# Optimization experiments

Measured on AMD Instinct MI355X. Metric: run time of the kernel, lower is better.

Reference implementation:

```python
import jax, jax.numpy as jnp
import numpy as np

N, D, E, R, G, M = 8192, 1024, 64, 64, 8, 8

def setup_inputs() -> dict:
    key = jax.random.key(0)
    k_h, k_wg, k_wl, k_w1, k_w2 = jax.random.split(key, 5)
    return {
        'h': jax.random.normal(k_h, (N, D), jnp.float32),
        'Wg': jax.random.normal(k_wg, (D, G), jnp.float32) * 0.02,  # nn.Linear weight (transposed)
        'bg': jnp.zeros((G,), jnp.float32),
        'Wloc': jax.random.normal(k_wl, (G, D, M), jnp.float32) * 0.02,
        'W1': jax.random.normal(k_w1, (E, D, R), jnp.float32) * 0.02,
        'W2': jax.random.normal(k_w2, (E, R, D), jnp.float32) * 0.02,
        'k': 2,
    }

def reference(h, Wg, bg, Wloc, W1, W2, k):
    n, d = h.shape
    g, _, m = Wloc.shape
    e = W1.shape[0]
    router_temp = 1.0
    # stage 1: group routing (top-1)
    g_scores = h @ Wg + bg                                   # (N, G)
    group_idx = jnp.argmax(g_scores, axis=-1)                # (N,)
    # stage 2: within-group scores; compute all groups (cheap: N*G*M) then select
    all_local = jnp.einsum('nd,gdm->ngm', h, Wloc)           # (N, G, M)
    local_scores = jnp.take_along_axis(all_local, group_idx[:, None, None], axis=1)[:, 0]  # (N, M)
    topv, topm = jax.lax.top_k(local_scores, k)              # (N, k)
    gate = jax.nn.softmax(topv / max(router_temp, 1e-6), axis=-1)
    expert_ids = group_idx[:, None] * m + topm               # (N, k) global expert ids
    # scatter gates into dense (N, E); topm entries are distinct per token
    gate_full = jnp.zeros((n, e), h.dtype).at[jnp.arange(n)[:, None], expert_ids].set(gate)
    # low-rank expert compute: relu(h @ W1) @ W2, weighted-combined
    tmp = jax.nn.relu(jnp.einsum('nd,edr->ner', h, W1))      # (N, E, R)
    out = jnp.einsum('ner,erd->nd', gate_full[:, :, None] * tmp, W2)  # (N, D)
    return out, expert_ids, gate, group_idx
```

## Files before the change

kernel.cpp:

```cpp
#include <hip/hip_runtime.h>
#include <hip/hip_bf16.h>
#include <cstdint>
#include <cstddef>

#define NTOK 8192
#define DIM  1024
#define NEXP 64
#define RANK 64
#define NGRP 8
#define NLOC 8

typedef __attribute__((ext_vector_type(8))) short bf16x8;
typedef __attribute__((ext_vector_type(4))) float f32x4;

static __device__ inline unsigned int pack_bf16x2(float a, float b) {
    __hip_bfloat16 ha = __float2bfloat16(a);
    __hip_bfloat16 hb = __float2bfloat16(b);
    return (unsigned int)(*(unsigned short*)&ha) |
           ((unsigned int)(*(unsigned short*)&hb) << 16);
}

__global__ __launch_bounds__(256, 2) void score_all(
    const float* __restrict__ h, const float* __restrict__ Wg,
    const float* __restrict__ Wloc, unsigned short* __restrict__ hb,
    float* __restrict__ Sp)
{
    __shared__ float Hs[64][65];
    __shared__ float Ws[64][44];

    const int tile = blockIdx.x;
    const int slab = blockIdx.y;
    const int z    = blockIdx.z;
    const int tid  = threadIdx.x;
    const int wave = tid >> 6;
    const int lane = tid & 63;
    const int t0   = tile * 64;
    const int kz   = z * 512;
    const int ncol = slab ? 32 : 40;

    float acc[10] = {};

    for (int chunk = 0; chunk < 8; ++chunk) {
        const int kb = kz + chunk * 64;
        __syncthreads();
        {
            const int r = tid >> 2, seg = (tid & 3) * 16;
            const float* src = h + (size_t)(t0 + r) * DIM + kb + seg;
            const float4 v0 = *(const float4*)(src);
            const float4 v1 = *(const float4*)(src + 4);
            const float4 v2 = *(const float4*)(src + 8);
            const float4 v3 = *(const float4*)(src + 12);
            float* dst = &Hs[r][seg];
            dst[0]  = v0.x; dst[1]  = v0.y; dst[2]  = v0.z; dst[3]  = v0.w;
            dst[4]  = v1.x; dst[5]  = v1.y; dst[6]  = v1.z; dst[7]  = v1.w;
            dst[8]  = v2.x; dst[9]  = v2.y; dst[10] = v2.z; dst[11] = v2.w;
            dst[12] = v3.x; dst[13] = v3.y; dst[14] = v3.z; dst[15] = v3.w;
            if (slab == 0) {
                unsigned short* hrow = hb + (size_t)(t0 + r) * DIM + kb + seg;
                uint2 p0, p1, p2, p3;
                p0.x = pack_bf16x2(v0.x, v0.y); p0.y = pack_bf16x2(v0.z, v0.w);
                p1.x = pack_bf16x2(v1.x, v1.y); p1.y = pack_bf16x2(v1.z, v1.w);
                p2.x = pack_bf16x2(v2.x, v2.y); p2.y = pack_bf16x2(v2.z, v2.w);
                p3.x = pack_bf16x2(v3.x, v3.y); p3.y = pack_bf16x2(v3.z, v3.w);
                *(uint2*)(hrow)      = p0;
                *(uint2*)(hrow + 4)  = p1;
                *(uint2*)(hrow + 8)  = p2;
                *(uint2*)(hrow + 12) = p3;
            }
        }
        {
            const int krow = tid & 63;
            const int c4b  = tid >> 6;
#pragma unroll
            for (int p = 0; p < 3; ++p) {
                const int c4 = c4b + p * 4;
                if (c4 * 4 < ncol) {
                    const int o = c4 >> 1, m4 = (c4 & 1) * 4;
                    const float* wsrc;
                    if (slab == 0) {
                        wsrc = (o == 0)
                            ? (Wg + (size_t)(kb + krow) * NGRP + m4)
                            : (Wloc + (size_t)(o - 1) * (DIM * NLOC)
                                    + (size_t)(kb + krow) * NLOC + m4);
                    } else {
                        wsrc = Wloc + (size_t)(4 + o) * (DIM * NLOC)
                                    + (size_t)(kb + krow) * NLOC + m4;
                    }
                    *(float4*)&Ws[krow][c4 * 4] = *(const float4*)wsrc;
                }
            }
        }
        __syncthreads();
        if (slab == 0) {
            const int c0 = wave * 10;
#pragma unroll 4
            for (int k = 0; k < 64; ++k) {
                const float a = Hs[lane][k];
                const float2 b0 = *(const float2*)&Ws[k][c0];
                const float2 b1 = *(const float2*)&Ws[k][c0 + 2];
                const float2 b2 = *(const float2*)&Ws[k][c0 + 4];
                const float2 b3 = *(const float2*)&Ws[k][c0 + 6];
                const float2 b4 = *(const float2*)&Ws[k][c0 + 8];
                acc[0] += a * b0.x; acc[1] += a * b0.y;
                acc[2] += a * b1.x; acc[3] += a * b1.y;
                acc[4] += a * b2.x; acc[5] += a * b2.y;
                acc[6] += a * b3.x; acc[7] += a * b3.y;
                acc[8] += a * b4.x; acc[9] += a * b4.y;
            }
        } else {
            const int c0 = wave * 8;
#pragma unroll 4
            for (int k = 0; k < 64; ++k) {
                const float a = Hs[lane][k];
                const float4 b0 = *(const float4*)&Ws[k][c0];
                const float4 b1 = *(const float4*)&Ws[k][c0 + 4];
                acc[0] += a * b0.x; acc[1] += a * b0.y;
                acc[2] += a * b0.z; acc[3] += a * b0.w;
                acc[4] += a * b1.x; acc[5] += a * b1.y;
                acc[6] += a * b1.z; acc[7] += a * b1.w;
            }
        }
    }
    const int gcol = (slab ? 40 + wave * 8 : wave * 10);
    float* dstS = Sp + (size_t)z * (NTOK * 72) + (size_t)(t0 + lane) * 72 + gcol;
    if (slab == 0) {
#pragma unroll
        for (int c = 0; c < 10; ++c) dstS[c] = acc[c];
    } else {
#pragma unroll
        for (int c = 0; c < 8; ++c) dstS[c] = acc[c];
    }
}

__global__ __launch_bounds__(256) void route_all(
    const float* __restrict__ Sp, const float* __restrict__ bg,
    float* __restrict__ out_gidx, float* __restrict__ out_eid,
    float* __restrict__ out_gate, int* __restrict__ ws_eids,
    float* __restrict__ ws_gates, int* __restrict__ counts_e)
{
    __shared__ int hist[NEXP];
    if (threadIdx.x < NEXP) hist[threadIdx.x] = 0;
    __syncthreads();

    const int t = blockIdx.x * 256 + threadIdx.x;
    const float* p0 = Sp + (size_t)t * 72;
    const float* p1 = Sp + (size_t)NTOK * 72 + (size_t)t * 72;
    float s[72];
#pragma unroll
    for (int i = 0; i < 18; ++i) {
        const float4 a = *(const float4*)(p0 + i * 4);
        const float4 b = *(const float4*)(p1 + i * 4);
        s[i * 4 + 0] = a.x + b.x; s[i * 4 + 1] = a.y + b.y;
        s[i * 4 + 2] = a.z + b.z; s[i * 4 + 3] = a.w + b.w;
    }

    int gi = 0; float best = s[0] + bg[0];
#pragma unroll
    for (int g = 1; g < NGRP; ++g) {
        const float v = s[g] + bg[g];
        if (v > best) { best = v; gi = g; }
    }

    float ls[NLOC];
#pragma unroll
    for (int m = 0; m < NLOC; ++m) ls[m] = s[8 + gi * NLOC + m];

    int m1 = 0; float v1 = ls[0];
#pragma unroll
    for (int m = 1; m < NLOC; ++m) { if (ls[m] > v1) { v1 = ls[m]; m1 = m; } }
    int m2 = (m1 == 0) ? 1 : 0; float v2 = ls[m2];
#pragma unroll
    for (int m = 0; m < NLOC; ++m) {
        if (m != m1 && m != ((m1 == 0) ? 1 : 0) && ls[m] > v2) { v2 = ls[m]; m2 = m; }
    }
    const float e2v = expf(v2 - v1);
    const float inv = 1.f / (1.f + e2v);
    const float g0 = inv, g1 = e2v * inv;
    const int ea = gi * NLOC + m1, eb = gi * NLOC + m2;

    out_gidx[t] = (float)gi;
    out_eid[t * 2 + 0] = (float)ea;
    out_eid[t * 2 + 1] = (float)eb;
    out_gate[t * 2 + 0] = g0;
    out_gate[t * 2 + 1] = g1;
    ws_eids[t * 2 + 0] = ea;
    ws_eids[t * 2 + 1] = eb;
    ws_gates[t * 2 + 0] = g0;
    ws_gates[t * 2 + 1] = g1;
    atomicAdd(&hist[ea], 1);
    atomicAdd(&hist[eb], 1);

    __syncthreads();
    if (threadIdx.x < NEXP) atomicAdd(&counts_e[threadIdx.x], hist[threadIdx.x]);
}

__global__ __launch_bounds__(256) void scatter_e(
    const int* __restrict__ ws_eids, const float* __restrict__ ws_gates,
    const int* __restrict__ counts_e, int* __restrict__ cursor,
    int* __restrict__ token_list, float* __restrict__ slot_gate)
{
    __shared__ int offS[64];
    const int tid = threadIdx.x;
    if (tid < 64) {
        const int c = counts_e[tid];
        int s = c;
#pragma unroll
        for (int d = 1; d < 64; d <<= 1) {
            int v = __shfl_up(s, d, 64);
            if (tid >= d) s += v;
        }
        offS[tid] = s - c;
    }
    __syncthreads();
    const int t = blockIdx.x * 256 + tid;
    if (t >= NTOK) return;
#pragma unroll
    for (int j = 0; j < 2; ++j) {
        const int eid = ws_eids[t * 2 + j];
        const int pos = offS[eid] + atomicAdd(&cursor[eid], 1);
        token_list[pos] = t * 2 + j;
        slot_gate[pos] = ws_gates[t * 2 + j];
    }
}

__global__ __launch_bounds__(256) void prep_w(
    const float* __restrict__ W1, const float* __restrict__ W2,
    unsigned short* __restrict__ W1t, unsigned short* __restrict__ W2t)
{
    __shared__ float Ls[64][65];
    const int e = blockIdx.x;
    const int y = blockIdx.y;
    if (y < 16) {
        const int kb = y;
        const float* src = W1 + (size_t)e * DIM * RANK + (size_t)kb * 64 * RANK;
#pragma unroll
        for (int it = 0; it < 4; ++it) {
            const int kk = (threadIdx.x >> 4) + it * 16;
            const int rr = (threadIdx.x & 15) * 4;
            *(float4*)&Ls[kk][rr] = *(const float4*)(src + (size_t)kk * RANK + rr);
        }
        __syncthreads();
#pragma unroll
        for (int it = 0; it < 2; ++it) {
            const int idx = threadIdx.x + it * 256;
            const int r = idx >> 3, k8 = (idx & 7) * 8;
            uint4 v;
            v.x = pack_bf16x2(Ls[k8 + 0][r], Ls[k8 + 1][r]);
            v.y = pack_bf16x2(Ls[k8 + 2][r], Ls[k8 + 3][r]);
            v.z = pack_bf16x2(Ls[k8 + 4][r], Ls[k8 + 5][r]);
            v.w = pack_bf16x2(Ls[k8 + 6][r], Ls[k8 + 7][r]);
            *(uint4*)(W1t + (size_t)e * RANK * DIM + (size_t)r * DIM + kb * 64 + k8) = v;
        }
    } else {
        const int db = y - 16;
        const float* src = W2 + (size_t)e * RANK * DIM + db * 64;
#pragma unroll
        for (int it = 0; it < 4; ++it) {
            const int rr = (threadIdx.x >> 4) + it * 16;
            const int dd = (threadIdx.x & 15) * 4;
            *(float4*)&Ls[rr][dd] = *(const float4*)(src + (size_t)rr * DIM + dd);
        }
        __syncthreads();
#pragma unroll
        for (int it = 0; it < 2; ++it) {
            const int idx = threadIdx.x + it * 256;
            const int d = idx >> 3, r8 = (idx & 7) * 8;
            uint4 v;
            v.x = pack_bf16x2(Ls[r8 + 0][d], Ls[r8 + 1][d]);
            v.y = pack_bf16x2(Ls[r8 + 2][d], Ls[r8 + 3][d]);
            v.z = pack_bf16x2(Ls[r8 + 4][d], Ls[r8 + 5][d]);
            v.w = pack_bf16x2(Ls[r8 + 6][d], Ls[r8 + 7][d]);
            *(uint4*)(W2t + (size_t)e * DIM * RANK + (size_t)(db * 64 + d) * RANK + r8) = v;
        }
    }
}

__global__ __launch_bounds__(256, 2) void e1_mfma(
    const unsigned short* __restrict__ hb, const unsigned short* __restrict__ W1t,
    const int* __restrict__ counts_e, const int* __restrict__ token_list,
    const float* __restrict__ slot_gate, unsigned short* __restrict__ P)
{
    __shared__ unsigned short Hs[64 * 72];
    __shared__ unsigned short Ws[64 * 72];
    __shared__ int   tokS[64];
    __shared__ float gateS[64];
    __shared__ int   offS[65];

    const int e   = blockIdx.x;
    const int tid = threadIdx.x;
    if (tid < 64) {
        const int c = counts_e[tid];
        int s = c;
#pragma unroll
        for (int d = 1; d < 64; d <<= 1) {
            int v = __shfl_up(s, d, 64);
            if (tid >= d) s += v;
        }
        offS[tid] = s - c;
        if (tid == 63) offS[64] = s;
    }
    __syncthreads();
    const int n0 = offS[e];
    const int ne = offS[e + 1] - n0;

    const unsigned short* W1te = W1t + (size_t)e * RANK * DIM;
    const int wave = tid >> 6;
    const int lane = tid & 63;
    const int tx   = lane & 15;
    const int quad = lane >> 4;

    for (int tile = blockIdx.y; tile * 64 < ne; tile += 8) {
        const int row0 = tile * 64;
        __syncthreads();
        if (tid < 64) {
            const int gr = row0 + tid;
            tokS[tid]  = (gr < ne) ? token_list[n0 + gr] : -1;
            gateS[tid] = (gr < ne) ? slot_gate[n0 + gr] : 0.f;
        }
        f32x4 acc[4] = {};
        for (int kc = 0; kc < DIM; kc += 64) {
            __syncthreads();
#pragma unroll
            for (int it = 0; it < 2; ++it) {
                const int idx = tid + it * 256;
                const int s = idx >> 3, k8 = (idx & 7) * 8;
                const int ent = tokS[s];
                uint4 v = make_uint4(0, 0, 0, 0);
                if (ent >= 0)
                    v = *(const uint4*)(hb + (size_t)(ent >> 1) * DIM + kc + k8);
                *(uint4*)(Hs + s * 72 + k8) = v;
            }
#pragma unroll
            for (int it = 0; it < 2; ++it) {
                const int idx = tid + it * 256;
                const int r = idx >> 3, k8 = (idx & 7) * 8;
                *(uint4*)(Ws + r * 72 + k8) =
                    *(const uint4*)(W1te + (size_t)r * DIM + kc + k8);
            }
            __syncthreads();
#pragma unroll
            for (int ks = 0; ks < 2; ++ks) {
                const bf16x8 a = *(const bf16x8*)(Hs + (wave * 16 + tx) * 72 + ks * 32 + quad * 8);
#pragma unroll
                for (int j = 0; j < 4; ++j) {
                    const bf16x8 b = *(const bf16x8*)(Ws + (j * 16 + tx) * 72 + ks * 32 + quad * 8);
                    acc[j] = __builtin_amdgcn_mfma_f32_16x16x32_bf16(a, b, acc[j], 0, 0, 0);
                }
            }
        }
#pragma unroll
        for (int j = 0; j < 4; ++j) {
#pragma unroll
            for (int i = 0; i < 4; ++i) {
                const int sl = wave * 16 + quad * 4 + i;
                const int gr = row0 + sl;
                if (gr < ne) {
                    const float v = fmaxf(acc[j][i], 0.f) * gateS[sl];
                    __hip_bfloat16 hv = __float2bfloat16(v);
                    P[(size_t)(n0 + gr) * RANK + j * 16 + tx] = *(unsigned short*)&hv;
                }
            }
        }
    }
}

__global__ __launch_bounds__(256, 2) void e2_mfma(
    const unsigned short* __restrict__ P, const unsigned short* __restrict__ W2t,
    const int* __restrict__ counts_e, const int* __restrict__ token_list,
    float* __restrict__ out, float* __restrict__ contrib)
{
    __shared__ unsigned short Ps[64 * 72];
    __shared__ unsigned short W2s[64 * 72];
    __shared__ int tokS[64];
    __shared__ int offS[65];

    const int e = blockIdx.x;
    const int colbase = blockIdx.y * 64;
    const int tid = threadIdx.x;
    if (tid < 64) {
        const int c = counts_e[tid];
        int s = c;
#pragma unroll
        for (int d = 1; d < 64; d <<= 1) {
            int v = __shfl_up(s, d, 64);
            if (tid >= d) s += v;
        }
        offS[tid] = s - c;
        if (tid == 63) offS[64] = s;
    }
    __syncthreads();
    const int n0 = offS[e];
    const int ne = offS[e + 1] - n0;

    const unsigned short* W2te = W2t + (size_t)e * DIM * RANK;
    const int wave = tid >> 6;
    const int lane = tid & 63;
    const int tx   = lane & 15;
    const int quad = lane >> 4;

#pragma unroll
    for (int it = 0; it < 2; ++it) {
        const int idx = tid + it * 256;
        const int d = idx >> 3, r8 = (idx & 7) * 8;
        *(uint4*)(W2s + d * 72 + r8) =
            *(const uint4*)(W2te + (size_t)(colbase + d) * RANK + r8);
    }

    for (int tile = blockIdx.z; tile * 64 < ne; tile += 4) {
        const int row0 = tile * 64;
        __syncthreads();
        if (tid < 64) {
            const int gr = row0 + tid;
            tokS[tid] = (gr < ne) ? token_list[n0 + gr] : -1;
        }
#pragma unroll
        for (int it = 0; it < 2; ++it) {
            const int idx = tid + it * 256;
            const int s = idx >> 3, r8 = (idx & 7) * 8;
            const int gr = row0 + s;
            uint4 v = make_uint4(0, 0, 0, 0);
            if (gr < ne) v = *(const uint4*)(P + (size_t)(n0 + gr) * RANK + r8);
            *(uint4*)(Ps + s * 72 + r8) = v;
        }
        __syncthreads();
        f32x4 acc[4] = {};
#pragma unroll
        for (int ks = 0; ks < 2; ++ks) {
            const bf16x8 a = *(const bf16x8*)(Ps + (wave * 16 + tx) * 72 + ks * 32 + quad * 8);
#pragma unroll
            for (int j = 0; j < 4; ++j) {
                const bf16x8 b = *(const bf16x8*)(W2s + (j * 16 + tx) * 72 + ks * 32 + quad * 8);
                acc[j] = __builtin_amdgcn_mfma_f32_16x16x32_bf16(a, b, acc[j], 0, 0, 0);
            }
        }
#pragma unroll
        for (int i = 0; i < 4; ++i) {
            const int sl = wave * 16 + quad * 4 + i;
            const int ent = tokS[sl];
            if (ent >= 0) {
                float* base = (ent & 1) ? contrib : out;
                float* op = base + (size_t)(ent >> 1) * DIM + colbase;
#pragma unroll
                for (int j = 0; j < 4; ++j)
                    op[j * 16 + tx] = acc[j][i];
            }
        }
    }
}

__global__ __launch_bounds__(256) void combine_kernel(
    const float* __restrict__ contrib, float* __restrict__ out)
{
    const size_t i = (size_t)blockIdx.x * 256 + threadIdx.x;
    float4 a = ((const float4*)out)[i];
    const float4 b = ((const float4*)contrib)[i];
    a.x += b.x; a.y += b.y; a.z += b.z; a.w += b.w;
    ((float4*)out)[i] = a;
}

extern "C" void kernel_launch(void* const* d_in, const int* in_sizes, int n_in,
                              void* d_out, int out_size, void* d_ws, size_t ws_size,
                              hipStream_t stream)
{
    const float* h    = (const float*)d_in[0];
    const float* Wg   = (const float*)d_in[1];
    const float* bg   = (const float*)d_in[2];
    const float* Wloc = (const float*)d_in[3];
    const float* W1   = (const float*)d_in[4];
    const float* W2   = (const float*)d_in[5];

    float* out_f    = (float*)d_out;
    float* out_main = out_f;
    float* out_eid  = out_f + (size_t)NTOK * DIM;
    float* out_gate = out_eid + (size_t)NTOK * 2;
    float* out_gidx = out_gate + (size_t)NTOK * 2;

    int* ws_i        = (int*)d_ws;
    int* counts_e    = ws_i;
    int* cursor_e    = ws_i + 192;
    int* ws_eids     = ws_i + 16896;
    int* token_list  = ws_i + 33280;
    float* ws_f      = (float*)(ws_i + 49664);
    float* ws_gates  = ws_f;
    float* slot_gate = ws_f + 16384;
    float* Sp        = ws_f + 2 * 16384;
    unsigned short* P_h = (unsigned short*)(Sp + (size_t)2 * NTOK * 72);
    unsigned short* W1t = P_h + (size_t)16384 * RANK;
    unsigned short* W2t = W1t + (size_t)NEXP * RANK * DIM;
    float* contrib      = (float*)(W2t + (size_t)NEXP * DIM * RANK);
    unsigned short* hb = (unsigned short*)contrib;

    hipMemsetAsync(ws_i, 0, 256 * sizeof(int), stream);

    prep_w<<<dim3(NEXP, 32), 256, 0, stream>>>(W1, W2, W1t, W2t);
    score_all<<<dim3(128, 2, 2), 256, 0, stream>>>(h, Wg, Wloc, hb, Sp);
    route_all<<<NTOK / 256, 256, 0, stream>>>(Sp, bg, out_gidx, out_eid,
        out_gate, ws_eids, ws_gates, counts_e);
    scatter_e<<<NTOK / 256, 256, 0, stream>>>(ws_eids, ws_gates, counts_e,
        cursor_e, token_list, slot_gate);
    e1_mfma<<<dim3(NEXP, 8), 256, 0, stream>>>(hb, W1t, counts_e, token_list,
        slot_gate, P_h);
    e2_mfma<<<dim3(NEXP, 16, 4), 256, 0, stream>>>(P_h, W2t, counts_e, token_list,
        out_main, contrib);
    combine_kernel<<<(NTOK * DIM / 4) / 256, 256, 0, stream>>>(contrib, out_main);
}
```

Before: 259.6 us.

## Double token tile in score kernel with register prefetch and transposed weight tile

The scoring kernel now handles 128 tokens per block instead of 64, so each weight value read from shared memory feeds two tokens. The weight tile is stored transposed so the inner loop reads four k values at once. The next chunk's h and weight values are prefetched into registers while the current chunk is computed. In exchange the grid has half as many blocks, register pressure rises (20 accumulators plus prefetch buffers), and the launch bound no longer asks for two blocks per CU, so occupancy may drop.

```diff
diff --git a/kernel.cpp b/kernel.cpp
--- a/kernel.cpp
+++ b/kernel.cpp
@@ -20,13 +20,13 @@
            ((unsigned int)(*(unsigned short*)&hb) << 16);
 }
 
-__global__ __launch_bounds__(256, 2) void score_all(
+__global__ __launch_bounds__(256) void score_all(
     const float* __restrict__ h, const float* __restrict__ Wg,
     const float* __restrict__ Wloc, unsigned short* __restrict__ hb,
     float* __restrict__ Sp)
 {
-    __shared__ float Hs[64][65];
-    __shared__ float Ws[64][44];
+    __shared__ float Hs[128][66];
+    __shared__ float Ws[40][72];
 
     const int tile = blockIdx.x;
     const int slab = blockIdx.y;
@@ -34,102 +34,207 @@
     const int tid  = threadIdx.x;
     const int wave = tid >> 6;
     const int lane = tid & 63;
-    const int t0   = tile * 64;
+    const int t0   = tile * 128;
     const int kz   = z * 512;
-    const int ncol = slab ? 32 : 40;
-
-    float acc[10] = {};
+
+    const int r0  = tid >> 2;
+    const int seg = (tid & 3) * 16;
+
+    float acc[20] = {};
+
+    float4 hpre[8];
+    float4 wgp;
+    float4 wlp[2];
+
+    {
+        const int kb = kz;
+#pragma unroll
+        for (int half = 0; half < 2; ++half) {
+            const float* src = h + (size_t)(t0 + half * 64 + r0) * DIM + kb + seg;
+            hpre[half * 4 + 0] = *(const float4*)(src);
+            hpre[half * 4 + 1] = *(const float4*)(src + 4);
+            hpre[half * 4 + 2] = *(const float4*)(src + 8);
+            hpre[half * 4 + 3] = *(const float4*)(src + 12);
+        }
+        if (slab == 0) {
+            if (tid < 128)
+                wgp = *(const float4*)(Wg + (size_t)(kb + (tid >> 1)) * NGRP + (tid & 1) * 4);
+#pragma unroll
+            for (int it = 0; it < 2; ++it) {
+                const int idx = tid + it * 256;
+                const int g = idx >> 7, r = idx & 127;
+                wlp[it] = *(const float4*)(Wloc + (size_t)g * (DIM * NLOC)
+                                               + (size_t)(kb + (r >> 1)) * NLOC + (r & 1) * 4);
+            }
+        } else {
+#pragma unroll
+            for (int it = 0; it < 2; ++it) {
+                const int idx = tid + it * 256;
+                const int g = idx >> 7, r = idx & 127;
+                wlp[it] = *(const float4*)(Wloc + (size_t)(4 + g) * (DIM * NLOC)
+                                               + (size_t)(kb + (r >> 1)) * NLOC + (r & 1) * 4);
+            }
+        }
+    }
 
     for (int chunk = 0; chunk < 8; ++chunk) {
         const int kb = kz + chunk * 64;
-        __syncthreads();
-        {
-            const int r = tid >> 2, seg = (tid & 3) * 16;
-            const float* src = h + (size_t)(t0 + r) * DIM + kb + seg;
-            const float4 v0 = *(const float4*)(src);
-            const float4 v1 = *(const float4*)(src + 4);
-            const float4 v2 = *(const float4*)(src + 8);
-            const float4 v3 = *(const float4*)(src + 12);
+
+#pragma unroll
+        for (int half = 0; half < 2; ++half) {
+            const int r = half * 64 + r0;
             float* dst = &Hs[r][seg];
-            dst[0]  = v0.x; dst[1]  = v0.y; dst[2]  = v0.z; dst[3]  = v0.w;
-            dst[4]  = v1.x; dst[5]  = v1.y; dst[6]  = v1.z; dst[7]  = v1.w;
-            dst[8]  = v2.x; dst[9]  = v2.y; dst[10] = v2.z; dst[11] = v2.w;
-            dst[12] = v3.x; dst[13] = v3.y; dst[14] = v3.z; dst[15] = v3.w;
+#pragma unroll
+            for (int q = 0; q < 4; ++q) {
+                const float4 v = hpre[half * 4 + q];
+                *(float2*)(dst + q * 4)     = make_float2(v.x, v.y);
+                *(float2*)(dst + q * 4 + 2) = make_float2(v.z, v.w);
+            }
             if (slab == 0) {
                 unsigned short* hrow = hb + (size_t)(t0 + r) * DIM + kb + seg;
-                uint2 p0, p1, p2, p3;
-                p0.x = pack_bf16x2(v0.x, v0.y); p0.y = pack_bf16x2(v0.z, v0.w);
-                p1.x = pack_bf16x2(v1.x, v1.y); p1.y = pack_bf16x2(v1.z, v1.w);
-                p2.x = pack_bf16x2(v2.x, v2.y); p2.y = pack_bf16x2(v2.z, v2.w);
-                p3.x = pack_bf16x2(v3.x, v3.y); p3.y = pack_bf16x2(v3.z, v3.w);
-                *(uint2*)(hrow)      = p0;
-                *(uint2*)(hrow + 4)  = p1;
-                *(uint2*)(hrow + 8)  = p2;
-                *(uint2*)(hrow + 12) = p3;
-            }
-        }
-        {
-            const int krow = tid & 63;
-            const int c4b  = tid >> 6;
-#pragma unroll
-            for (int p = 0; p < 3; ++p) {
-                const int c4 = c4b + p * 4;
-                if (c4 * 4 < ncol) {
-                    const int o = c4 >> 1, m4 = (c4 & 1) * 4;
-                    const float* wsrc;
-                    if (slab == 0) {
-                        wsrc = (o == 0)
-                            ? (Wg + (size_t)(kb + krow) * NGRP + m4)
-                            : (Wloc + (size_t)(o - 1) * (DIM * NLOC)
-                                    + (size_t)(kb + krow) * NLOC + m4);
-                    } else {
-                        wsrc = Wloc + (size_t)(4 + o) * (DIM * NLOC)
-                                    + (size_t)(kb + krow) * NLOC + m4;
-                    }
-                    *(float4*)&Ws[krow][c4 * 4] = *(const float4*)wsrc;
-                }
+#pragma unroll
+                for (int q = 0; q < 4; ++q) {
+                    const float4 v = hpre[half * 4 + q];
+                    uint2 pk;
+                    pk.x = pack_bf16x2(v.x, v.y);
+                    pk.y = pack_bf16x2(v.z, v.w);
+                    *(uint2*)(hrow + q * 4) = pk;
+                }
+            }
+        }
+        if (slab == 0) {
+            if (tid < 128) {
+                const int k = tid >> 1, m4 = (tid & 1) * 4;
+                Ws[m4 + 0][k] = wgp.x; Ws[m4 + 1][k] = wgp.y;
+                Ws[m4 + 2][k] = wgp.z; Ws[m4 + 3][k] = wgp.w;
+            }
+#pragma unroll
+            for (int it = 0; it < 2; ++it) {
+                const int idx = tid + it * 256;
+                const int g = idx >> 7, r = idx & 127;
+                const int k = r >> 1, c = 8 + g * 8 + (r & 1) * 4;
+                const float4 v = wlp[it];
+                Ws[c + 0][k] = v.x; Ws[c + 1][k] = v.y;
+                Ws[c + 2][k] = v.z; Ws[c + 3][k] = v.w;
+            }
+        } else {
+#pragma unroll
+            for (int it = 0; it < 2; ++it) {
+                const int idx = tid + it * 256;
+                const int g = idx >> 7, r = idx & 127;
+                const int k = r >> 1, c = g * 8 + (r & 1) * 4;
+                const float4 v = wlp[it];
+                Ws[c + 0][k] = v.x; Ws[c + 1][k] = v.y;
+                Ws[c + 2][k] = v.z; Ws[c + 3][k] = v.w;
             }
         }
         __syncthreads();
+
+        if (chunk < 7) {
+            const int kbn = kb + 64;
+#pragma unroll
+            for (int half = 0; half < 2; ++half) {
+                const float* src = h + (size_t)(t0 + half * 64 + r0) * DIM + kbn + seg;
+                hpre[half * 4 + 0] = *(const float4*)(src);
+                hpre[half * 4 + 1] = *(const float4*)(src + 4);
+                hpre[half * 4 + 2] = *(const float4*)(src + 8);
+                hpre[half * 4 + 3] = *(const float4*)(src + 12);
+            }
+            if (slab == 0) {
+                if (tid < 128)
+                    wgp = *(const float4*)(Wg + (size_t)(kbn + (tid >> 1)) * NGRP + (tid & 1) * 4);
+#pragma unroll
+                for (int it = 0; it < 2; ++it) {
+                    const int idx = tid + it * 256;
+                    const int g = idx >> 7, r = idx & 127;
+                    wlp[it] = *(const float4*)(Wloc + (size_t)g * (DIM * NLOC)
+                                                   + (size_t)(kbn + (r >> 1)) * NLOC + (r & 1) * 4);
+                }
+            } else {
+#pragma unroll
+                for (int it = 0; it < 2; ++it) {
+                    const int idx = tid + it * 256;
+                    const int g = idx >> 7, r = idx & 127;
+                    wlp[it] = *(const float4*)(Wloc + (size_t)(4 + g) * (DIM * NLOC)
+                                                   + (size_t)(kbn + (r >> 1)) * NLOC + (r & 1) * 4);
+                }
+            }
+        }
+
         if (slab == 0) {
             const int c0 = wave * 10;
-#pragma unroll 4
-            for (int k = 0; k < 64; ++k) {
-                const float a = Hs[lane][k];
-                const float2 b0 = *(const float2*)&Ws[k][c0];
-                const float2 b1 = *(const float2*)&Ws[k][c0 + 2];
-                const float2 b2 = *(const float2*)&Ws[k][c0 + 4];
-                const float2 b3 = *(const float2*)&Ws[k][c0 + 6];
-                const float2 b4 = *(const float2*)&Ws[k][c0 + 8];
-                acc[0] += a * b0.x; acc[1] += a * b0.y;
-                acc[2] += a * b1.x; acc[3] += a * b1.y;
-                acc[4] += a * b2.x; acc[5] += a * b2.y;
-                acc[6] += a * b3.x; acc[7] += a * b3.y;
-                acc[8] += a * b4.x; acc[9] += a * b4.y;
+#pragma unroll 2
+            for (int kq = 0; kq < 16; ++kq) {
+                const int k0 = kq * 4;
+                const float2 a00 = *(const float2*)&Hs[lane][k0];
+                const float2 a01 = *(const float2*)&Hs[lane][k0 + 2];
+                const float2 a10 = *(const float2*)&Hs[64 + lane][k0];
+                const float2 a11 = *(const float2*)&Hs[64 + lane][k0 + 2];
+                float4 bq[10];
+#pragma unroll
+                for (int c = 0; c < 10; ++c)
+                    bq[c] = *(const float4*)&Ws[c0 + c][k0];
+#pragma unroll
+                for (int c = 0; c < 10; ++c) {
+                    acc[c] += a00.x * bq[c].x; acc[10 + c] += a10.x * bq[c].x;
+                }
+#pragma unroll
+                for (int c = 0; c < 10; ++c) {
+                    acc[c] += a00.y * bq[c].y; acc[10 + c] += a10.y * bq[c].y;
+                }
+#pragma unroll
+                for (int c = 0; c < 10; ++c) {
+                    acc[c] += a01.x * bq[c].z; acc[10 + c] += a11.x * bq[c].z;
+                }
+#pragma unroll
+                for (int c = 0; c < 10; ++c) {
+                    acc[c] += a01.y * bq[c].w; acc[10 + c] += a11.y * bq[c].w;
+                }
             }
         } else {
             const int c0 = wave * 8;
-#pragma unroll 4
-            for (int k = 0; k < 64; ++k) {
-                const float a = Hs[lane][k];
-                const float4 b0 = *(const float4*)&Ws[k][c0];
-                const float4 b1 = *(const float4*)&Ws[k][c0 + 4];
-                acc[0] += a * b0.x; acc[1] += a * b0.y;
-                acc[2] += a * b0.z; acc[3] += a * b0.w;
-                acc[4] += a * b1.x; acc[5] += a * b1.y;
-                acc[6] += a * b1.z; acc[7] += a * b1.w;
-            }
-        }
-    }
+#pragma unroll 2
+            for (int kq = 0; kq < 16; ++kq) {
+                const int k0 = kq * 4;
+                const float2 a00 = *(const float2*)&Hs[lane][k0];
+                const float2 a01 = *(const float2*)&Hs[lane][k0 + 2];
+                const float2 a10 = *(const float2*)&Hs[64 + lane][k0];
+                const float2 a11 = *(const float2*)&Hs[64 + lane][k0 + 2];
+                float4 bq[8];
+#pragma unroll
+                for (int c = 0; c < 8; ++c)
+                    bq[c] = *(const float4*)&Ws[c0 + c][k0];
+#pragma unroll
+                for (int c = 0; c < 8; ++c) {
+                    acc[c] += a00.x * bq[c].x; acc[10 + c] += a10.x * bq[c].x;
+                }
+#pragma unroll
+                for (int c = 0; c < 8; ++c) {
+                    acc[c] += a00.y * bq[c].y; acc[10 + c] += a10.y * bq[c].y;
+                }
+#pragma unroll
+                for (int c = 0; c < 8; ++c) {
+                    acc[c] += a01.x * bq[c].z; acc[10 + c] += a11.x * bq[c].z;
+                }
+#pragma unroll
+                for (int c = 0; c < 8; ++c) {
+                    acc[c] += a01.y * bq[c].w; acc[10 + c] += a11.y * bq[c].w;
+                }
+            }
+        }
+        __syncthreads();
+    }
+
     const int gcol = (slab ? 40 + wave * 8 : wave * 10);
+    const int nout = slab ? 8 : 10;
     float* dstS = Sp + (size_t)z * (NTOK * 72) + (size_t)(t0 + lane) * 72 + gcol;
-    if (slab == 0) {
-#pragma unroll
-        for (int c = 0; c < 10; ++c) dstS[c] = acc[c];
-    } else {
-#pragma unroll
-        for (int c = 0; c < 8; ++c) dstS[c] = acc[c];
-    }
+#pragma unroll
+    for (int c = 0; c < 10; ++c)
+        if (c < nout) dstS[c] = acc[c];
+    float* dstS2 = Sp + (size_t)z * (NTOK * 72) + (size_t)(t0 + 64 + lane) * 72 + gcol;
+#pragma unroll
+    for (int c = 0; c < 10; ++c)
+        if (c < nout) dstS2[c] = acc[10 + c];
 }
 
 __global__ __launch_bounds__(256) void route_all(
@@ -144,7 +249,7 @@
 
     const int t = blockIdx.x * 256 + threadIdx.x;
     const float* p0 = Sp + (size_t)t * 72;
-    const float* p1 = Sp + (size_t)NTOK * 72 + (size_t)t * 72;
+    const float* p1 = p0 + (size_t)NTOK * 72;
     float s[72];
 #pragma unroll
     for (int i = 0; i < 18; ++i) {
@@ -493,7 +598,7 @@
     hipMemsetAsync(ws_i, 0, 256 * sizeof(int), stream);
 
     prep_w<<<dim3(NEXP, 32), 256, 0, stream>>>(W1, W2, W1t, W2t);
-    score_all<<<dim3(128, 2, 2), 256, 0, stream>>>(h, Wg, Wloc, hb, Sp);
+    score_all<<<dim3(64, 2, 2), 256, 0, stream>>>(h, Wg, Wloc, hb, Sp);
     route_all<<<NTOK / 256, 256, 0, stream>>>(Sp, bg, out_gidx, out_eid,
         out_gate, ws_eids, ws_gates, counts_e);
     scatter_e<<<NTOK / 256, 256, 0, stream>>>(ws_eids, ws_gates, counts_e,
```

Result: no change. 254.7 us (-1.9%).
